# Performance work log

Measured on AMD Instinct MI355X. Metric: run time of the kernel, lower is better.

Reference implementation:

```python
import jax, jax.numpy as jnp
import numpy as np

NUM_HEADS = 8
NUM_POINTS = 4


def setup_inputs() -> dict:
    key = jax.random.key(0)
    bs, h, w = 2, 128, 128
    cin = cout = 256
    nq = h * w
    ks = jax.random.split(key, 6)
    query = jax.random.normal(ks[0], (bs, nq, cin), jnp.float32)
    value = jax.random.normal(ks[1], (bs, nq, cin), jnp.float32)
    # sampling_offsets: small random weight, bias = directional grid init (as in init_weights)
    W_off = jax.random.normal(ks[2], (cin, NUM_HEADS * NUM_POINTS * 2), jnp.float32) * 0.01
    thetas = np.arange(NUM_HEADS, dtype=np.float32) * (2.0 * np.pi / NUM_HEADS)
    grid = np.stack([np.cos(thetas), np.sin(thetas)], -1)
    grid = grid / np.abs(grid).max(-1, keepdims=True)
    grid = np.tile(grid[:, None, :], (1, NUM_POINTS, 1)) * (np.arange(NUM_POINTS, dtype=np.float32)[None, :, None] + 1.0)
    b_off = jnp.asarray(grid.reshape(-1), jnp.float32)
    W_attn = jax.random.normal(ks[3], (cin, NUM_HEADS * NUM_POINTS), jnp.float32) * 0.01
    b_attn = jnp.zeros((NUM_HEADS * NUM_POINTS,), jnp.float32)
    s = 1.0 / np.sqrt(cin)  # xavier-ish uniform
    W_val = jax.random.uniform(ks[4], (cin, cout), jnp.float32, -s, s)
    b_val = jnp.zeros((cout,), jnp.float32)
    W_out = jax.random.uniform(ks[5], (cout, cout), jnp.float32, -s, s)
    b_out = jnp.zeros((cout,), jnp.float32)
    return {"query": query, "value": value, "W_off": W_off, "b_off": b_off,
            "W_attn": W_attn, "b_attn": b_attn, "W_val": W_val, "b_val": b_val,
            "W_out": W_out, "b_out": b_out, "h": h, "w": w}


def _bilinear_sample(v_flat, ix, iy, h, w):
    # v_flat: (bs, heads, h*w, d); ix/iy: (bs, heads, nq, P) pixel coords.
    # grid_sample bilinear, align_corners=False, padding_mode='zeros'.
    x0 = jnp.floor(ix)
    y0 = jnp.floor(iy)
    wx1 = ix - x0
    wy1 = iy - y0
    bs, hd, nq, P = ix.shape
    acc = 0.0
    corners = ((x0, y0, (1.0 - wx1) * (1.0 - wy1)),
               (x0 + 1.0, y0, wx1 * (1.0 - wy1)),
               (x0, y0 + 1.0, (1.0 - wx1) * wy1),
               (x0 + 1.0, y0 + 1.0, wx1 * wy1))
    for xc, yc, wgt in corners:
        xi = xc.astype(jnp.int32)
        yi = yc.astype(jnp.int32)
        valid = (xi >= 0) & (xi < w) & (yi >= 0) & (yi < h)
        idx = jnp.clip(yi, 0, h - 1) * w + jnp.clip(xi, 0, w - 1)
        g = jnp.take_along_axis(v_flat, idx.reshape(bs, hd, nq * P)[..., None], axis=2)
        acc = acc + g.reshape(bs, hd, nq, P, -1) * (wgt * valid)[..., None]
    return acc  # (bs, heads, nq, P, d)


def deform_attn(query, value, W_off, b_off, W_attn, b_attn, W_val, b_val, h, w):
    bs, nq, _ = query.shape
    d = W_val.shape[1] // NUM_HEADS
    v = (value @ W_val + b_val).reshape(bs, nq, NUM_HEADS, d)
    off = (query @ W_off + b_off).reshape(bs, nq, NUM_HEADS, NUM_POINTS, 2)
    aw = jax.nn.softmax((query @ W_attn + b_attn).reshape(bs, nq, NUM_HEADS, NUM_POINTS), axis=-1)
    # reference points in [0,1], scale_ratio=1.0, (x, y) order
    ys = (jnp.arange(h, dtype=jnp.float32) + 0.5) / h
    xs = (jnp.arange(w, dtype=jnp.float32) + 0.5) / w
    ry, rx = jnp.meshgrid(ys, xs, indexing='ij')
    ref = jnp.stack([rx.reshape(-1), ry.reshape(-1)], -1)  # (nq, 2)
    loc = ref[None, :, None, None, :] + off / jnp.array([w, h], jnp.float32)
    grid = 2.0 * loc - 1.0  # normalized grid_sample coords
    grid = grid.transpose(0, 2, 1, 3, 4)  # (bs, heads, nq, P, 2)
    ix = (grid[..., 0] + 1.0) * (w / 2.0) - 0.5
    iy = (grid[..., 1] + 1.0) * (h / 2.0) - 0.5
    v_flat = v.transpose(0, 2, 1, 3)  # (bs, heads, h*w, d)
    sampled = _bilinear_sample(v_flat, ix, iy, h, w)  # (bs, heads, nq, P, d)
    out = (sampled * aw.transpose(0, 2, 1, 3)[..., None]).sum(3)  # (bs, heads, nq, d)
    return out.transpose(0, 2, 1, 3).reshape(bs, nq, NUM_HEADS * d)


def reference(query, value, W_off, b_off, W_attn, b_attn, W_val, b_val, W_out, b_out, h, w):
    attn = deform_attn(query, value, W_off, b_off, W_attn, b_attn, W_val, b_val, h, w)
    # dropout acts as identity in eval mode; identity residual = query
    return attn @ W_out + b_out + query
```

## Files before the change

### kernel.cpp

```cpp
#include <hip/hip_runtime.h>

#define H_IMG 128
#define W_IMG 128
#define NQ (H_IMG * W_IMG)
#define CIN 256
#define NH 8
#define NP 4
#define DH 32
#define LDSP 264

typedef __bf16 bf16x4 __attribute__((ext_vector_type(4)));
typedef __bf16 bf16x8 __attribute__((ext_vector_type(8)));
typedef _Float16 f16x8 __attribute__((ext_vector_type(8)));
typedef float f32x4 __attribute__((ext_vector_type(4)));

__global__ __launch_bounds__(256) void prep_weights(
    const float* __restrict__ Wval, const float* __restrict__ Wout,
    const float* __restrict__ Woff, const float* __restrict__ Wattn,
    const float* __restrict__ boff, const float* __restrict__ battn,
    __bf16* __restrict__ btv, _Float16* __restrict__ bto,
    __bf16* __restrict__ btoa, float* __restrict__ bias96) {
  int id = blockIdx.x * 256 + threadIdx.x;
  if (id < 256 * 256) {
    int n = id >> 8, k = id & 255;
    btv[n * 256 + k] = (__bf16)Wval[k * 256 + n];
    bto[n * 256 + k] = (_Float16)Wout[k * 256 + n];
  }
  if (id < 96 * 256) {
    int n = id >> 8, k = id & 255;
    float w = (n < 64) ? Woff[k * 64 + n] : Wattn[k * 32 + (n - 64)];
    btoa[n * 256 + k] = (__bf16)w;
  }
  if (id < 96) {
    bias96[id] = (id < 64) ? boff[id] : battn[id - 64];
  }
}

__global__ __launch_bounds__(256) void gemm_v(
    const float* __restrict__ A, const __bf16* __restrict__ BT,
    const float* __restrict__ bias, _Float16* __restrict__ v, int M) {
  const int t = threadIdx.x;
  const int lane = t & 63;
  const int wave = t >> 6;
  const int r = lane & 15;
  const int q = lane >> 4;
  const int gm0 = blockIdx.x * 64;
  const int wn = wave * 64;

  __shared__ __bf16 As[64 * LDSP];

#pragma unroll
  for (int i = 0; i < 16; ++i) {
    int g = i * 256 + t;
    int row = g >> 6, c4 = g & 63;
    float4 f = *(const float4*)(A + (size_t)(gm0 + row) * 256 + c4 * 4);
    bf16x4 hh;
    hh[0] = (__bf16)f.x; hh[1] = (__bf16)f.y;
    hh[2] = (__bf16)f.z; hh[3] = (__bf16)f.w;
    *(bf16x4*)(&As[row * LDSP + c4 * 4]) = hh;
  }
  __syncthreads();

  f32x4 acc[4][4];
#pragma unroll
  for (int mt = 0; mt < 4; ++mt)
#pragma unroll
    for (int nt = 0; nt < 4; ++nt) acc[mt][nt] = (f32x4){0.f, 0.f, 0.f, 0.f};

#pragma unroll
  for (int kt = 0; kt < 8; ++kt) {
    const int ko = kt * 32 + q * 8;
    bf16x8 a[4], b[4];
#pragma unroll
    for (int mt = 0; mt < 4; ++mt)
      a[mt] = *(const bf16x8*)(&As[(mt * 16 + r) * LDSP + ko]);
#pragma unroll
    for (int nt = 0; nt < 4; ++nt)
      b[nt] = *(const bf16x8*)(BT + (size_t)(wn + nt * 16 + r) * 256 + ko);
#pragma unroll
    for (int mt = 0; mt < 4; ++mt)
#pragma unroll
      for (int nt = 0; nt < 4; ++nt)
        acc[mt][nt] =
            __builtin_amdgcn_mfma_f32_16x16x32_bf16(a[mt], b[nt], acc[mt][nt], 0, 0, 0);
  }

#pragma unroll
  for (int mt = 0; mt < 4; ++mt)
#pragma unroll
    for (int nt = 0; nt < 4; ++nt)
#pragma unroll
      for (int rr = 0; rr < 4; ++rr) {
        int row = gm0 + mt * 16 + q * 4 + rr;
        int col = wn + nt * 16 + r;
        v[((size_t)(col >> 5) * M + row) * 32 + (col & 31)] =
            (_Float16)(acc[mt][nt][rr] + bias[col]);
      }
}

__global__ __launch_bounds__(256, 2) void oa_sample_out(
    const float* __restrict__ query, const __bf16* __restrict__ btoa,
    const float* __restrict__ bias96, const _Float16* __restrict__ v,
    const _Float16* __restrict__ bto, const float* __restrict__ b_out,
    float* __restrict__ out, int M) {
  const int t = threadIdx.x;
  const int lane = t & 63;
  const int wave = t >> 6;
  const int r = lane & 15;
  const int q = lane >> 4;
  const int gm0 = blockIdx.x * 64;

  __shared__ __bf16 As[64 * LDSP];
  __shared__ float oas[64 * 100];
  _Float16* Asf = (_Float16*)As;

#pragma unroll
  for (int i = 0; i < 16; ++i) {
    int g = i * 256 + t;
    int row = g >> 6, c4 = g & 63;
    float4 f = *(const float4*)(query + (size_t)(gm0 + row) * 256 + c4 * 4);
    bf16x4 hh;
    hh[0] = (__bf16)f.x; hh[1] = (__bf16)f.y;
    hh[2] = (__bf16)f.z; hh[3] = (__bf16)f.w;
    *(bf16x4*)(&As[row * LDSP + c4 * 4]) = hh;
  }

  float resid[4][4][4];
#pragma unroll
  for (int mt = 0; mt < 4; ++mt)
#pragma unroll
    for (int nt = 0; nt < 4; ++nt)
#pragma unroll
      for (int rr = 0; rr < 4; ++rr)
        resid[mt][nt][rr] =
            query[(size_t)(gm0 + mt * 16 + q * 4 + rr) * 256 + wave * 64 + nt * 16 + r];

  __syncthreads();

  {
    const int wm = (wave & 1) * 32;
    const int n0 = (wave >> 1) * 48;
    f32x4 acc[2][3];
#pragma unroll
    for (int mt = 0; mt < 2; ++mt)
#pragma unroll
      for (int nt = 0; nt < 3; ++nt) acc[mt][nt] = (f32x4){0.f, 0.f, 0.f, 0.f};
#pragma unroll
    for (int kt = 0; kt < 8; ++kt) {
      const int ko = kt * 32 + q * 8;
      bf16x8 a0 = *(const bf16x8*)(&As[(wm + r) * LDSP + ko]);
      bf16x8 a1 = *(const bf16x8*)(&As[(wm + 16 + r) * LDSP + ko]);
      bf16x8 b[3];
#pragma unroll
      for (int nt = 0; nt < 3; ++nt)
        b[nt] = *(const bf16x8*)(btoa + (size_t)(n0 + nt * 16 + r) * 256 + ko);
#pragma unroll
      for (int nt = 0; nt < 3; ++nt) {
        acc[0][nt] = __builtin_amdgcn_mfma_f32_16x16x32_bf16(a0, b[nt], acc[0][nt], 0, 0, 0);
        acc[1][nt] = __builtin_amdgcn_mfma_f32_16x16x32_bf16(a1, b[nt], acc[1][nt], 0, 0, 0);
      }
    }
#pragma unroll
    for (int mt = 0; mt < 2; ++mt)
#pragma unroll
      for (int nt = 0; nt < 3; ++nt)
#pragma unroll
        for (int rr = 0; rr < 4; ++rr) {
          int rl = wm + mt * 16 + q * 4 + rr;
          int col = n0 + nt * 16 + r;
          oas[rl * 100 + col] = acc[mt][nt][rr] + bias96[col];
        }
  }
  __syncthreads();

  {
    const int qrow = t >> 2;
    const int c8 = (t & 3) * 8;
    const int row = gm0 + qrow;
    const int b = row >> 14;
    const int qi = row & (NQ - 1);
    const int x = qi & (W_IMG - 1);
    const int y = qi >> 7;
    const float* oar = &oas[qrow * 100];
#pragma unroll
    for (int h = 0; h < NH; ++h) {
      float l0 = oar[64 + h * 4 + 0];
      float l1 = oar[64 + h * 4 + 1];
      float l2 = oar[64 + h * 4 + 2];
      float l3 = oar[64 + h * 4 + 3];
      float mx = fmaxf(fmaxf(l0, l1), fmaxf(l2, l3));
      float e0 = __expf(l0 - mx), e1 = __expf(l1 - mx);
      float e2 = __expf(l2 - mx), e3 = __expf(l3 - mx);
      float inv = 1.f / (e0 + e1 + e2 + e3);
      float awp[4] = {e0 * inv, e1 * inv, e2 * inv, e3 * inv};

      int offs[16];
      float wvs[16];
#pragma unroll
      for (int p = 0; p < NP; ++p) {
        float ox = oar[h * 8 + p * 2 + 0];
        float oy = oar[h * 8 + p * 2 + 1];
        float ix = (float)x + ox;
        float iy = (float)y + oy;
        float x0f = floorf(ix), y0f = floorf(iy);
        float wx1 = ix - x0f, wy1 = iy - y0f;
        int x0 = (int)x0f, y0 = (int)y0f;
        float wgt[4] = {(1.f - wx1) * (1.f - wy1), wx1 * (1.f - wy1),
                        (1.f - wx1) * wy1, wx1 * wy1};
        int xs[4] = {x0, x0 + 1, x0, x0 + 1};
        int ysv[4] = {y0, y0, y0 + 1, y0 + 1};
#pragma unroll
        for (int c = 0; c < 4; ++c) {
          int xi = xs[c], yi = ysv[c];
          bool valid = (xi >= 0) & (xi < W_IMG) & (yi >= 0) & (yi < H_IMG);
          int xc = xi < 0 ? 0 : (xi > W_IMG - 1 ? W_IMG - 1 : xi);
          int yc = yi < 0 ? 0 : (yi > H_IMG - 1 ? H_IMG - 1 : yi);
          offs[p * 4 + c] = (yc * W_IMG + xc) * (DH * 2);
          wvs[p * 4 + c] = awp[p] * wgt[c] * (valid ? 1.f : 0.f);
        }
      }

      const char* vb =
          (const char*)v + ((size_t)h * M + (size_t)b * NQ) * (DH * 2) + c8 * 2;
      f16x8 g[16];
#pragma unroll
      for (int i = 0; i < 16; ++i) g[i] = *(const f16x8*)(vb + offs[i]);

      f16x8 fa = {};
#pragma unroll
      for (int i = 0; i < 16; ++i) fa += g[i] * (_Float16)wvs[i];

      *(f16x8*)(&Asf[qrow * LDSP + h * DH + c8]) = fa;
    }
  }
  __syncthreads();

  {
    const int wn = wave * 64;
    f32x4 acc[4][4];
#pragma unroll
    for (int mt = 0; mt < 4; ++mt)
#pragma unroll
      for (int nt = 0; nt < 4; ++nt) acc[mt][nt] = (f32x4){0.f, 0.f, 0.f, 0.f};
#pragma unroll
    for (int kt = 0; kt < 8; ++kt) {
      const int ko = kt * 32 + q * 8;
      f16x8 a[4], b[4];
#pragma unroll
      for (int mt = 0; mt < 4; ++mt)
        a[mt] = *(const f16x8*)(&Asf[(mt * 16 + r) * LDSP + ko]);
#pragma unroll
      for (int nt = 0; nt < 4; ++nt)
        b[nt] = *(const f16x8*)(bto + (size_t)(wn + nt * 16 + r) * 256 + ko);
#pragma unroll
      for (int mt = 0; mt < 4; ++mt)
#pragma unroll
        for (int nt = 0; nt < 4; ++nt)
          acc[mt][nt] =
              __builtin_amdgcn_mfma_f32_16x16x32_f16(a[mt], b[nt], acc[mt][nt], 0, 0, 0);
    }
#pragma unroll
    for (int mt = 0; mt < 4; ++mt)
#pragma unroll
      for (int nt = 0; nt < 4; ++nt)
#pragma unroll
        for (int rr = 0; rr < 4; ++rr) {
          int row = gm0 + mt * 16 + q * 4 + rr;
          int col = wn + nt * 16 + r;
          out[(size_t)row * 256 + col] =
              acc[mt][nt][rr] + b_out[col] + resid[mt][nt][rr];
        }
  }
}

extern "C" void kernel_launch(void* const* d_in, const int* in_sizes, int n_in,
                              void* d_out, int out_size, void* d_ws, size_t ws_size,
                              hipStream_t stream) {
  const float* query  = (const float*)d_in[0];
  const float* value  = (const float*)d_in[1];
  const float* W_off  = (const float*)d_in[2];
  const float* b_off  = (const float*)d_in[3];
  const float* W_attn = (const float*)d_in[4];
  const float* b_attn = (const float*)d_in[5];
  const float* W_val  = (const float*)d_in[6];
  const float* b_val  = (const float*)d_in[7];
  const float* W_out  = (const float*)d_in[8];
  const float* b_out  = (const float*)d_in[9];
  float* out = (float*)d_out;

  char* ws = (char*)d_ws;
  __bf16*   btv    = (__bf16*)(ws + 0);
  _Float16* bto    = (_Float16*)(ws + 131072);
  __bf16*   btoa   = (__bf16*)(ws + 262144);
  float*    bias96 = (float*)(ws + 311296);
  _Float16* v      = (_Float16*)(ws + 524288);

  const int M = in_sizes[0] / CIN;

  prep_weights<<<256, 256, 0, stream>>>(W_val, W_out, W_off, W_attn,
                                        b_off, b_attn, btv, bto, btoa, bias96);
  gemm_v<<<M / 64, 256, 0, stream>>>(value, btv, b_val, v, M);
  oa_sample_out<<<M / 64, 256, 0, stream>>>(query, btoa, bias96, v, bto, b_out, out, M);
}
```

Baseline: 164.5 us.

## Double fused sampling kernel block size to 512 threads with redistributed work

The fused offset/attention GEMM, sampling and output-projection kernel now launches 512 threads per 64-row block instead of 256. Each phase is re-partitioned: the offset GEMM uses 16-row wave tiles, sampling splits the 8 heads into two groups of 4 per thread, and the output GEMM uses 32x64 wave tiles. The aim is more waves per block to hide gather latency and shorter serial per-thread work. The cost is halved per-wave reuse of B fragments in the GEMMs and possible register pressure under the new launch bounds.

New measurement: 173.1 us. 1.05x slower.

```diff
diff --git a/kernel.cpp b/kernel.cpp
--- a/kernel.cpp
+++ b/kernel.cpp
@@ -98,7 +98,7 @@
       }
 }
 
-__global__ __launch_bounds__(256, 2) void oa_sample_out(
+__global__ __launch_bounds__(512, 2) void oa_sample_out(
     const float* __restrict__ query, const __bf16* __restrict__ btoa,
     const float* __restrict__ bias96, const _Float16* __restrict__ v,
     const _Float16* __restrict__ bto, const float* __restrict__ b_out,
@@ -115,8 +115,8 @@
   _Float16* Asf = (_Float16*)As;
 
 #pragma unroll
-  for (int i = 0; i < 16; ++i) {
-    int g = i * 256 + t;
+  for (int i = 0; i < 8; ++i) {
+    int g = i * 512 + t;
     int row = g >> 6, c4 = g & 63;
     float4 f = *(const float4*)(query + (size_t)(gm0 + row) * 256 + c4 * 4);
     bf16x4 hh;
@@ -125,56 +125,53 @@
     *(bf16x4*)(&As[row * LDSP + c4 * 4]) = hh;
   }
 
-  float resid[4][4][4];
-#pragma unroll
-  for (int mt = 0; mt < 4; ++mt)
+  const int p4_wm = (wave & 1) * 32;
+  const int p4_wn = (wave >> 1) * 64;
+  float resid[2][4][4];
+#pragma unroll
+  for (int mt = 0; mt < 2; ++mt)
 #pragma unroll
     for (int nt = 0; nt < 4; ++nt)
 #pragma unroll
       for (int rr = 0; rr < 4; ++rr)
         resid[mt][nt][rr] =
-            query[(size_t)(gm0 + mt * 16 + q * 4 + rr) * 256 + wave * 64 + nt * 16 + r];
+            query[(size_t)(gm0 + p4_wm + mt * 16 + q * 4 + rr) * 256 + p4_wn + nt * 16 + r];
 
   __syncthreads();
 
   {
-    const int wm = (wave & 1) * 32;
-    const int n0 = (wave >> 1) * 48;
-    f32x4 acc[2][3];
-#pragma unroll
-    for (int mt = 0; mt < 2; ++mt)
-#pragma unroll
-      for (int nt = 0; nt < 3; ++nt) acc[mt][nt] = (f32x4){0.f, 0.f, 0.f, 0.f};
+    const int wm = (wave & 3) * 16;
+    const int n0 = (wave >> 2) * 48;
+    f32x4 acc[3];
+#pragma unroll
+    for (int nt = 0; nt < 3; ++nt) acc[nt] = (f32x4){0.f, 0.f, 0.f, 0.f};
 #pragma unroll
     for (int kt = 0; kt < 8; ++kt) {
       const int ko = kt * 32 + q * 8;
-      bf16x8 a0 = *(const bf16x8*)(&As[(wm + r) * LDSP + ko]);
-      bf16x8 a1 = *(const bf16x8*)(&As[(wm + 16 + r) * LDSP + ko]);
+      bf16x8 a = *(const bf16x8*)(&As[(wm + r) * LDSP + ko]);
       bf16x8 b[3];
 #pragma unroll
       for (int nt = 0; nt < 3; ++nt)
         b[nt] = *(const bf16x8*)(btoa + (size_t)(n0 + nt * 16 + r) * 256 + ko);
 #pragma unroll
-      for (int nt = 0; nt < 3; ++nt) {
-        acc[0][nt] = __builtin_amdgcn_mfma_f32_16x16x32_bf16(a0, b[nt], acc[0][nt], 0, 0, 0);
-        acc[1][nt] = __builtin_amdgcn_mfma_f32_16x16x32_bf16(a1, b[nt], acc[1][nt], 0, 0, 0);
+      for (int nt = 0; nt < 3; ++nt)
+        acc[nt] = __builtin_amdgcn_mfma_f32_16x16x32_bf16(a, b[nt], acc[nt], 0, 0, 0);
+    }
+#pragma unroll
+    for (int nt = 0; nt < 3; ++nt)
+#pragma unroll
+      for (int rr = 0; rr < 4; ++rr) {
+        int rl = wm + q * 4 + rr;
+        int col = n0 + nt * 16 + r;
+        oas[rl * 100 + col] = acc[nt][rr] + bias96[col];
       }
-    }
-#pragma unroll
-    for (int mt = 0; mt < 2; ++mt)
-#pragma unroll
-      for (int nt = 0; nt < 3; ++nt)
-#pragma unroll
-        for (int rr = 0; rr < 4; ++rr) {
-          int rl = wm + mt * 16 + q * 4 + rr;
-          int col = n0 + nt * 16 + r;
-          oas[rl * 100 + col] = acc[mt][nt][rr] + bias96[col];
-        }
   }
   __syncthreads();
 
   {
-    const int qrow = t >> 2;
+    const int slot = t >> 2;
+    const int qrow = slot & 63;
+    const int hgrp = slot >> 6;
     const int c8 = (t & 3) * 8;
     const int row = gm0 + qrow;
     const int b = row >> 14;
@@ -183,7 +180,8 @@
     const int y = qi >> 7;
     const float* oar = &oas[qrow * 100];
 #pragma unroll
-    for (int h = 0; h < NH; ++h) {
+    for (int hh_ = 0; hh_ < 4; ++hh_) {
+      const int h = hgrp * 4 + hh_;
       float l0 = oar[64 + h * 4 + 0];
       float l1 = oar[64 + h * 4 + 1];
       float l2 = oar[64 + h * 4 + 2];
@@ -236,37 +234,36 @@
   __syncthreads();
 
   {
-    const int wn = wave * 64;
-    f32x4 acc[4][4];
-#pragma unroll
-    for (int mt = 0; mt < 4; ++mt)
+    f32x4 acc[2][4];
+#pragma unroll
+    for (int mt = 0; mt < 2; ++mt)
 #pragma unroll
       for (int nt = 0; nt < 4; ++nt) acc[mt][nt] = (f32x4){0.f, 0.f, 0.f, 0.f};
 #pragma unroll
     for (int kt = 0; kt < 8; ++kt) {
       const int ko = kt * 32 + q * 8;
-      f16x8 a[4], b[4];
-#pragma unroll
-      for (int mt = 0; mt < 4; ++mt)
-        a[mt] = *(const f16x8*)(&Asf[(mt * 16 + r) * LDSP + ko]);
+      f16x8 a[2], b[4];
+#pragma unroll
+      for (int mt = 0; mt < 2; ++mt)
+        a[mt] = *(const f16x8*)(&Asf[(p4_wm + mt * 16 + r) * LDSP + ko]);
 #pragma unroll
       for (int nt = 0; nt < 4; ++nt)
-        b[nt] = *(const f16x8*)(bto + (size_t)(wn + nt * 16 + r) * 256 + ko);
-#pragma unroll
-      for (int mt = 0; mt < 4; ++mt)
+        b[nt] = *(const f16x8*)(bto + (size_t)(p4_wn + nt * 16 + r) * 256 + ko);
+#pragma unroll
+      for (int mt = 0; mt < 2; ++mt)
 #pragma unroll
         for (int nt = 0; nt < 4; ++nt)
           acc[mt][nt] =
               __builtin_amdgcn_mfma_f32_16x16x32_f16(a[mt], b[nt], acc[mt][nt], 0, 0, 0);
     }
 #pragma unroll
-    for (int mt = 0; mt < 4; ++mt)
+    for (int mt = 0; mt < 2; ++mt)
 #pragma unroll
       for (int nt = 0; nt < 4; ++nt)
 #pragma unroll
         for (int rr = 0; rr < 4; ++rr) {
-          int row = gm0 + mt * 16 + q * 4 + rr;
-          int col = wn + nt * 16 + r;
+          int row = gm0 + p4_wm + mt * 16 + q * 4 + rr;
+          int col = p4_wn + nt * 16 + r;
           out[(size_t)row * 256 + col] =
               acc[mt][nt][rr] + b_out[col] + resid[mt][nt][rr];
         }
@@ -300,5 +297,5 @@
   prep_weights<<<256, 256, 0, stream>>>(W_val, W_out, W_off, W_attn,
                                         b_off, b_attn, btv, bto, btoa, bias96);
   gemm_v<<<M / 64, 256, 0, stream>>>(value, btv, b_val, v, M);
-  oa_sample_out<<<M / 64, 256, 0, stream>>>(query, btoa, bias96, v, bto, b_out, out, M);
+  oa_sample_out<<<M / 64, 512, 0, stream>>>(query, btoa, bias96, v, bto, b_out, out, M);
 }
```
